# Kernel optimization log

Measured on AMD Instinct MI355X. Metric: run time of the kernel, lower is better.

Reference implementation:

```python
import jax, jax.numpy as jnp
import numpy as np

TOPK_FRAC = 0.05
TOPK_MIN = 5
TOPK_MAX = 64


def setup_inputs() -> dict:
    key = jax.random.key(0)
    ks = jax.random.split(key, 8)
    N, H, B = 131072, 256, 512
    x = jax.random.normal(ks[0], (N, H), dtype=jnp.float32)
    batch = jnp.sort(jax.random.randint(ks[1], (N,), 0, B, dtype=jnp.int32))
    W1 = jax.random.normal(ks[2], (H, H // 2), dtype=jnp.float32) * 0.05
    b1 = jax.random.normal(ks[3], (H // 2,), dtype=jnp.float32) * 0.05
    W2 = jax.random.normal(ks[4], (H // 2, 1), dtype=jnp.float32) * 0.05
    b2 = jax.random.normal(ks[5], (1,), dtype=jnp.float32) * 0.05
    Wf = jax.random.normal(ks[6], (4 * H, H), dtype=jnp.float32) * 0.05
    bf = jax.random.normal(ks[7], (H,), dtype=jnp.float32) * 0.05
    return {"x": x, "batch": batch, "W1": W1, "b1": b1, "W2": W2,
            "b2": b2, "Wf": Wf, "bf": bf, "num_graphs": B}


def _forward(x, batch, W1, b1, W2, b2, Wf, bf, B):
    N = x.shape[0]
    # attention scores per node: MLP -> scalar
    s = (jax.nn.relu(x @ W1 + b1) @ W2 + b2)[:, 0]  # [N]
    # pyg_softmax: segment-wise stable softmax over nodes of each graph
    seg_max = jax.ops.segment_max(s, batch, num_segments=B)
    seg_max = jnp.where(jnp.isfinite(seg_max), seg_max, 0.0)  # guard empty segs
    e = jnp.exp(s - seg_max[batch])
    denom = jax.ops.segment_sum(e, batch, num_segments=B)
    w = e / denom[batch]                                    # [N]
    # pools
    x_attn = jax.ops.segment_sum(x * w[:, None], batch, num_segments=B)
    counts = jax.ops.segment_sum(jnp.ones((N,), jnp.int32), batch, num_segments=B)
    cnt_f = jnp.maximum(counts, 1).astype(x.dtype)
    x_mean = jax.ops.segment_sum(x, batch, num_segments=B) / cnt_f[:, None]
    x_max = jax.ops.segment_max(x, batch, num_segments=B)
    x_max = jnp.where(counts[:, None] > 0, x_max, 0.0)
    # per-graph dynamic k
    n = counts
    k = jnp.maximum(TOPK_MIN, jnp.ceil(TOPK_FRAC * n.astype(jnp.float32)).astype(jnp.int32))
    k = jnp.minimum(jnp.minimum(k, TOPK_MAX), n)            # [B]
    # fused segment top-k mean: sort nodes by (batch asc, w desc), keep rank<k
    order = jnp.lexsort((-w, batch))
    starts = jnp.concatenate([jnp.zeros((1,), jnp.int32), jnp.cumsum(counts)[:-1].astype(jnp.int32)])
    bs = batch[order]
    rank = jnp.arange(N, dtype=jnp.int32) - starts[bs]
    sel = (rank < k[bs]).astype(x.dtype)
    x_topk = jax.ops.segment_sum(x[order] * sel[:, None], bs, num_segments=B)
    x_topk = x_topk / jnp.maximum(k, 1).astype(x.dtype)[:, None]
    g = jax.nn.relu(jnp.concatenate([x_mean, x_attn, x_max, x_topk], axis=1) @ Wf + bf)
    return g


def reference(x, batch, W1, b1, W2, b2, Wf, bf, num_graphs):
    return _forward(x, batch, W1, b1, W2, b2, Wf, bf, num_graphs)
```

## Files before the change

kernel.cpp:

```cpp
#include <hip/hip_runtime.h>
#include <math.h>

#define H 256
#define HH 128
#define B_GRAPHS 512

typedef __attribute__((ext_vector_type(8))) short bfrag8;
typedef __attribute__((ext_vector_type(16))) float f32x16;

__global__ void k_prep_w1(const float* __restrict__ W1, ushort* __restrict__ W1b) {
  const int idx = blockIdx.x * 256 + threadIdx.x;
  const int k = idx >> 7, c = idx & 127;
  const float v = W1[idx];
  const uint u = __builtin_bit_cast(uint, v);
  const float r = v - __builtin_bit_cast(float, u & 0xFFFF0000u);
  const int base = (((k >> 4) * 2 + ((k >> 3) & 1)) * 128 + c) * 8 + (k & 7);
  W1b[base] = (ushort)(u >> 16);
  W1b[32768 + base] = (ushort)(__builtin_bit_cast(uint, r) >> 16);
}

__global__ void k_seg_bounds(const int* __restrict__ batch, int* __restrict__ seg_start,
                             int N, int B) {
  int b = blockIdx.x * blockDim.x + threadIdx.x;
  if (b > B) return;
  int lo = 0, hi = N;
  while (lo < hi) {
    int mid = (lo + hi) >> 1;
    if (batch[mid] < b) lo = mid + 1; else hi = mid;
  }
  seg_start[b] = lo;
}

__device__ __forceinline__ void splitbf(const float4 v0, const float4 v1,
                                        bfrag8& a0, bfrag8& a1) {
  const float vals[8] = {v0.x, v0.y, v0.z, v0.w, v1.x, v1.y, v1.z, v1.w};
#pragma unroll
  for (int e = 0; e < 8; ++e) {
    const uint u = __builtin_bit_cast(uint, vals[e]);
    a0[e] = (short)(u >> 16);
    const float r = vals[e] - __builtin_bit_cast(float, u & 0xFFFF0000u);
    a1[e] = (short)(__builtin_bit_cast(uint, r) >> 16);
  }
}

__global__ __launch_bounds__(256, 3) void k_score_mfma(
    const float* __restrict__ x, const ushort* __restrict__ W1b,
    const float* __restrict__ b1, const float* __restrict__ W2,
    const float* __restrict__ b2, float* __restrict__ s_out) {
  __shared__ float xs[4][2192];
  const int t = threadIdx.x;
  const int lane = t & 63;
  const int w = t >> 6;
  const int nl = lane & 31, g = lane >> 5;
  const int chunk = blockIdx.x * 4 + w;
  const int node0 = chunk * 32;
  float* myxs = &xs[w][0];

  f32x16 acc[4];
  acc[0] = (f32x16)0.f; acc[1] = (f32x16)0.f;
  acc[2] = (f32x16)0.f; acc[3] = (f32x16)0.f;

  const int lrow = lane >> 4;
  const int lcol = lane & 15;
  const float* gsrc = x + (size_t)(node0 + lrow) * H + lcol * 4;

  float4 gx[8];
#pragma unroll
  for (int q = 0; q < 8; ++q)
    gx[q] = *(const float4*)(gsrc + (size_t)(q * 4) * H);

#pragma unroll
  for (int ks = 0; ks < 4; ++ks) {
#pragma unroll
    for (int q = 0; q < 8; ++q)
      *(float4*)&myxs[(q * 4 + lrow) * 68 + lcol * 4] = gx[q];
    if (ks < 3) {
#pragma unroll
      for (int q = 0; q < 8; ++q)
        gx[q] = *(const float4*)(gsrc + (size_t)(q * 4) * H + (ks + 1) * 64);
    }
#pragma unroll
    for (int sub = 0; sub < 4; ++sub) {
      const int kks = ks * 4 + sub;
      const float4 v0 = *(const float4*)&myxs[nl * 68 + sub * 16 + g * 8];
      const float4 v1 = *(const float4*)&myxs[nl * 68 + sub * 16 + g * 8 + 4];
      bfrag8 a0, a1;
      splitbf(v0, v1, a0, a1);
#pragma unroll
      for (int j = 0; j < 4; ++j) {
        const ushort* bp = W1b + (size_t)((kks * 2 + g) * 128 + j * 32 + nl) * 8;
        const bfrag8 b0 = *(const bfrag8*)bp;
        const bfrag8 b1f = *(const bfrag8*)(bp + 32768);
        acc[j] = __builtin_amdgcn_mfma_f32_32x32x16_bf16(a0, b0, acc[j], 0, 0, 0);
        acc[j] = __builtin_amdgcn_mfma_f32_32x32x16_bf16(a0, b1f, acc[j], 0, 0, 0);
        acc[j] = __builtin_amdgcn_mfma_f32_32x32x16_bf16(a1, b0, acc[j], 0, 0, 0);
      }
    }
  }

  float b1v[4], w2v[4];
#pragma unroll
  for (int j = 0; j < 4; ++j) {
    b1v[j] = b1[j * 32 + nl];
    w2v[j] = W2[j * 32 + nl];
  }
  float p[16];
#pragma unroll
  for (int r = 0; r < 16; ++r) {
    float v = 0.f;
#pragma unroll
    for (int j = 0; j < 4; ++j)
      v = fmaf(fmaxf(acc[j][r] + b1v[j], 0.f), w2v[j], v);
#pragma unroll
    for (int m = 1; m <= 16; m <<= 1) v += __shfl_xor(v, m);
    p[r] = v;
  }
  if (nl == 0) {
    const float bb = b2[0];
#pragma unroll
    for (int r = 0; r < 16; ++r) {
      const int row = (r & 3) + 8 * (r >> 2) + 4 * g;
      s_out[node0 + row] = p[r] + bb;
    }
  }
}

__global__ __launch_bounds__(512) void k_pool_fused(const float* __restrict__ x,
                                                    const float* __restrict__ s,
                                                    const int* __restrict__ seg_start,
                                                    float* __restrict__ pooled) {
  const int b = blockIdx.x;
  const int t = threadIdx.x;
  const int start = seg_start[b];
  const int end = seg_start[b + 1];
  const int n = end - start;

  __shared__ float s_lds[1024];
  __shared__ float red[512];
  __shared__ float thr_sh;
  __shared__ int thri_sh;
  __shared__ float r4[8][264];

  const bool fits = (n <= 1024);
  if (fits) {
    for (int i = t; i < n; i += 512) s_lds[i] = s[start + i];
  }
  __syncthreads();
  const float* sseg = fits ? s_lds : (s + start);

  float m = -INFINITY;
  for (int i = t; i < n; i += 512) m = fmaxf(m, sseg[i]);
  red[t] = m;
  __syncthreads();
  for (int off = 256; off > 0; off >>= 1) {
    if (t < off) red[t] = fmaxf(red[t], red[t + off]);
    __syncthreads();
  }
  const float smax = red[0];
  __syncthreads();
  float d = 0.f;
  for (int i = t; i < n; i += 512) d += __expf(sseg[i] - smax);
  red[t] = d;
  __syncthreads();
  for (int off = 256; off > 0; off >>= 1) {
    if (t < off) red[t] += red[t + off];
    __syncthreads();
  }
  const float denom = red[0];
  __syncthreads();
  const float inv_denom = (denom > 0.f) ? 1.f / denom : 0.f;

  int k = 0;
  if (n > 0) {
    k = (int)ceilf(0.05f * (float)n);
    if (k < 5) k = 5;
    if (k > 64) k = 64;
    if (k > n) k = n;
  }

  if (t < 64) {
    float pk = INFINITY;
    int pidx = -1;
    for (int r = 0; r < k; ++r) {
      float bk = -INFINITY;
      int bi = 0x7fffffff;
      for (int i = t; i < n; i += 64) {
        const float si = sseg[i];
        const int gi = start + i;
        const bool below = (si < pk) || (si == pk && gi > pidx);
        if (below && (si > bk || (si == bk && gi < bi))) { bk = si; bi = gi; }
      }
#pragma unroll
      for (int off = 32; off > 0; off >>= 1) {
        const float ok = __shfl_xor(bk, off);
        const int oi = __shfl_xor(bi, off);
        if (ok > bk || (ok == bk && oi < bi)) { bk = ok; bi = oi; }
      }
      pk = bk;
      pidx = bi;
    }
    if (t == 0) {
      thr_sh = (k > 0) ? pk : INFINITY;
      thri_sh = (k > 0) ? pidx : -1;
    }
  }
  __syncthreads();
  const float thr = thr_sh;
  const int thri = thri_sh;

  const int fq = t & 63;
  const int sub = t >> 6;
  float mean[4] = {0.f, 0.f, 0.f, 0.f};
  float attn[4] = {0.f, 0.f, 0.f, 0.f};
  float tk[4] = {0.f, 0.f, 0.f, 0.f};
  float mx[4] = {-INFINITY, -INFINITY, -INFINITY, -INFINITY};
  for (int i = sub; i < n; i += 8) {
    const float si = sseg[i];
    const float wi = __expf(si - smax);
    const int gi = start + i;
    const bool sel = (si > thr) || (si == thr && gi <= thri);
    const float4 xv = *reinterpret_cast<const float4*>(x + (size_t)gi * H + fq * 4);
    mean[0] += xv.x; mean[1] += xv.y; mean[2] += xv.z; mean[3] += xv.w;
    attn[0] = fmaf(xv.x, wi, attn[0]);
    attn[1] = fmaf(xv.y, wi, attn[1]);
    attn[2] = fmaf(xv.z, wi, attn[2]);
    attn[3] = fmaf(xv.w, wi, attn[3]);
    mx[0] = fmaxf(mx[0], xv.x);
    mx[1] = fmaxf(mx[1], xv.y);
    mx[2] = fmaxf(mx[2], xv.z);
    mx[3] = fmaxf(mx[3], xv.w);
    if (sel) {
      tk[0] += xv.x; tk[1] += xv.y; tk[2] += xv.z; tk[3] += xv.w;
    }
  }
  float* po = pooled + (size_t)b * 1024;
  const float invn = 1.f / (float)(n > 0 ? n : 1);
  const float invk = (k > 0) ? 1.f / (float)k : 0.f;
  *reinterpret_cast<float4*>(&r4[sub][fq * 4]) = make_float4(mean[0], mean[1], mean[2], mean[3]);
  __syncthreads();
  if (t < 256) {
    float tot = 0.f;
#pragma unroll
    for (int q = 0; q < 8; ++q) tot += r4[q][t];
    po[t] = tot * invn;
  }
  __syncthreads();
  *reinterpret_cast<float4*>(&r4[sub][fq * 4]) = make_float4(attn[0], attn[1], attn[2], attn[3]);
  __syncthreads();
  if (t < 256) {
    float tot = 0.f;
#pragma unroll
    for (int q = 0; q < 8; ++q) tot += r4[q][t];
    po[256 + t] = tot * inv_denom;
  }
  __syncthreads();
  *reinterpret_cast<float4*>(&r4[sub][fq * 4]) = make_float4(mx[0], mx[1], mx[2], mx[3]);
  __syncthreads();
  if (t < 256) {
    float tot = -INFINITY;
#pragma unroll
    for (int q = 0; q < 8; ++q) tot = fmaxf(tot, r4[q][t]);
    po[512 + t] = (n > 0) ? tot : 0.f;
  }
  __syncthreads();
  *reinterpret_cast<float4*>(&r4[sub][fq * 4]) = make_float4(tk[0], tk[1], tk[2], tk[3]);
  __syncthreads();
  if (t < 256) {
    float tot = 0.f;
#pragma unroll
    for (int q = 0; q < 8; ++q) tot += r4[q][t];
    po[768 + t] = tot * invk;
  }
}

__global__ __launch_bounds__(256) void k_gemm(const float* __restrict__ pooled,
                                              const float* __restrict__ Wf,
                                              float* __restrict__ gacc) {
  const int t = threadIdx.x;
  const int r0 = blockIdx.x * 8;
  const int kc0 = blockIdx.y * 128;
  __shared__ float ps[8][132];
  {
    const int r = t >> 5;
    const int c = (t & 31) << 2;
    *reinterpret_cast<float4*>(&ps[r][c]) =
        *reinterpret_cast<const float4*>(pooled + (size_t)(r0 + r) * 1024 + kc0 + c);
  }
  __syncthreads();
  float acc[8];
#pragma unroll
  for (int r = 0; r < 8; ++r) acc[r] = 0.f;
#pragma unroll 4
  for (int c = 0; c < 128; ++c) {
    const float wf = Wf[(size_t)(kc0 + c) * 256 + t];
#pragma unroll
    for (int r = 0; r < 8; ++r) acc[r] = fmaf(ps[r][c], wf, acc[r]);
  }
  float* go = gacc + ((size_t)blockIdx.y * B_GRAPHS + r0) * 256;
#pragma unroll
  for (int r = 0; r < 8; ++r) go[r * 256 + t] = acc[r];
}

__global__ __launch_bounds__(256) void k_out(const float* __restrict__ gacc,
                                             const float* __restrict__ bf,
                                             float* __restrict__ out) {
  const int i = blockIdx.x * 256 + threadIdx.x;
  float v = bf[i & 255];
#pragma unroll
  for (int ks = 0; ks < 8; ++ks) v += gacc[(size_t)ks * (B_GRAPHS * 256) + i];
  out[i] = fmaxf(v, 0.f);
}

extern "C" void kernel_launch(void* const* d_in, const int* in_sizes, int n_in,
                              void* d_out, int out_size, void* d_ws, size_t ws_size,
                              hipStream_t stream) {
  const float* x  = (const float*)d_in[0];
  const int* batch = (const int*)d_in[1];
  const float* W1 = (const float*)d_in[2];
  const float* b1 = (const float*)d_in[3];
  const float* W2 = (const float*)d_in[4];
  const float* b2 = (const float*)d_in[5];
  const float* Wf = (const float*)d_in[6];
  const float* bf = (const float*)d_in[7];
  const int N = in_sizes[1];
  const int B = B_GRAPHS;

  float* ws = (float*)d_ws;
  float* s = ws;
  int* seg_start = (int*)(ws + N);
  float* pooled = ws + N + 1024;
  float* gacc = pooled + (size_t)B * 1024;
  ushort* W1b = (ushort*)(gacc + (size_t)8 * B * 256);

  k_prep_w1<<<dim3(128), dim3(256), 0, stream>>>(W1, W1b);
  k_seg_bounds<<<dim3((B + 1 + 255) / 256), dim3(256), 0, stream>>>(batch, seg_start, N, B);
  k_score_mfma<<<dim3(N / 128), dim3(256), 0, stream>>>(x, W1b, b1, W2, b2, s);
  k_pool_fused<<<dim3(B), dim3(512), 0, stream>>>(x, s, seg_start, pooled);
  k_gemm<<<dim3(B / 8, 8), dim3(256), 0, stream>>>(pooled, Wf, gacc);
  k_out<<<dim3((B * 256) / 256), dim3(256), 0, stream>>>(gacc, bf, (float*)d_out);
}
```

Baseline: 110.4 us.

## Split score GEMM K-dimension across warps with LDS partial-sum reduction

The score kernel previously gave each wavefront 32 nodes and looped over the full K=256, staging x through shared memory. Now each block handles 32 nodes and its four wavefronts each take a quarter of K, loading x directly into registers. The partial accumulators are then reduced through shared memory before the ReLU/W2 epilogue. This gives four times more blocks and shorter per-wave dependency chains, at the cost of extra LDS traffic and two block barriers.

```diff
diff --git a/kernel.cpp b/kernel.cpp
--- a/kernel.cpp
+++ b/kernel.cpp
@@ -47,81 +47,81 @@
     const float* __restrict__ x, const ushort* __restrict__ W1b,
     const float* __restrict__ b1, const float* __restrict__ W2,
     const float* __restrict__ b2, float* __restrict__ s_out) {
-  __shared__ float xs[4][2192];
+  __shared__ float part[4][16][128];
   const int t = threadIdx.x;
   const int lane = t & 63;
   const int w = t >> 6;
   const int nl = lane & 31, g = lane >> 5;
-  const int chunk = blockIdx.x * 4 + w;
-  const int node0 = chunk * 32;
-  float* myxs = &xs[w][0];
+  const int node0 = blockIdx.x * 32;
 
   f32x16 acc[4];
   acc[0] = (f32x16)0.f; acc[1] = (f32x16)0.f;
   acc[2] = (f32x16)0.f; acc[3] = (f32x16)0.f;
 
-  const int lrow = lane >> 4;
-  const int lcol = lane & 15;
-  const float* gsrc = x + (size_t)(node0 + lrow) * H + lcol * 4;
-
-  float4 gx[8];
-#pragma unroll
-  for (int q = 0; q < 8; ++q)
-    gx[q] = *(const float4*)(gsrc + (size_t)(q * 4) * H);
-
-#pragma unroll
-  for (int ks = 0; ks < 4; ++ks) {
-#pragma unroll
-    for (int q = 0; q < 8; ++q)
-      *(float4*)&myxs[(q * 4 + lrow) * 68 + lcol * 4] = gx[q];
-    if (ks < 3) {
-#pragma unroll
-      for (int q = 0; q < 8; ++q)
-        gx[q] = *(const float4*)(gsrc + (size_t)(q * 4) * H + (ks + 1) * 64);
-    }
-#pragma unroll
-    for (int sub = 0; sub < 4; ++sub) {
-      const int kks = ks * 4 + sub;
-      const float4 v0 = *(const float4*)&myxs[nl * 68 + sub * 16 + g * 8];
-      const float4 v1 = *(const float4*)&myxs[nl * 68 + sub * 16 + g * 8 + 4];
-      bfrag8 a0, a1;
-      splitbf(v0, v1, a0, a1);
-#pragma unroll
-      for (int j = 0; j < 4; ++j) {
-        const ushort* bp = W1b + (size_t)((kks * 2 + g) * 128 + j * 32 + nl) * 8;
-        const bfrag8 b0 = *(const bfrag8*)bp;
-        const bfrag8 b1f = *(const bfrag8*)(bp + 32768);
-        acc[j] = __builtin_amdgcn_mfma_f32_32x32x16_bf16(a0, b0, acc[j], 0, 0, 0);
-        acc[j] = __builtin_amdgcn_mfma_f32_32x32x16_bf16(a0, b1f, acc[j], 0, 0, 0);
-        acc[j] = __builtin_amdgcn_mfma_f32_32x32x16_bf16(a1, b0, acc[j], 0, 0, 0);
+  const float* gsrc = x + (size_t)(node0 + nl) * H + w * 64 + g * 8;
+  float4 xv[4][2];
+#pragma unroll
+  for (int sub = 0; sub < 4; ++sub) {
+    xv[sub][0] = *(const float4*)(gsrc + sub * 16);
+    xv[sub][1] = *(const float4*)(gsrc + sub * 16 + 4);
+  }
+
+#pragma unroll
+  for (int sub = 0; sub < 4; ++sub) {
+    const int kks = w * 4 + sub;
+    bfrag8 a0, a1;
+    splitbf(xv[sub][0], xv[sub][1], a0, a1);
+#pragma unroll
+    for (int j = 0; j < 4; ++j) {
+      const ushort* bp = W1b + (size_t)((kks * 2 + g) * 128 + j * 32 + nl) * 8;
+      const bfrag8 b0 = *(const bfrag8*)bp;
+      const bfrag8 b1f = *(const bfrag8*)(bp + 32768);
+      acc[j] = __builtin_amdgcn_mfma_f32_32x32x16_bf16(a0, b0, acc[j], 0, 0, 0);
+      acc[j] = __builtin_amdgcn_mfma_f32_32x32x16_bf16(a0, b1f, acc[j], 0, 0, 0);
+      acc[j] = __builtin_amdgcn_mfma_f32_32x32x16_bf16(a1, b0, acc[j], 0, 0, 0);
+    }
+  }
+
+  const float b2v = b2[0];
+  const int hb = (t & 15) * 8;
+  const int nloc = t >> 4;
+  float b1q[8], w2q[8];
+#pragma unroll
+  for (int e = 0; e < 8; ++e) {
+    b1q[e] = b1[hb + e];
+    w2q[e] = W2[hb + e];
+  }
+
+#pragma unroll
+  for (int P = 0; P < 2; ++P) {
+#pragma unroll
+    for (int j = 0; j < 4; ++j)
+#pragma unroll
+      for (int rr = 0; rr < 8; ++rr) {
+        const int nd = (rr & 3) + 8 * (rr >> 2) + 4 * g;
+        part[w][nd][j * 32 + nl] = acc[j][P * 8 + rr];
       }
-    }
-  }
-
-  float b1v[4], w2v[4];
-#pragma unroll
-  for (int j = 0; j < 4; ++j) {
-    b1v[j] = b1[j * 32 + nl];
-    w2v[j] = W2[j * 32 + nl];
-  }
-  float p[16];
-#pragma unroll
-  for (int r = 0; r < 16; ++r) {
+    __syncthreads();
+    float h8[8];
+#pragma unroll
+    for (int e = 0; e < 8; e += 4) {
+      const float4 s0 = *(const float4*)&part[0][nloc][hb + e];
+      const float4 s1 = *(const float4*)&part[1][nloc][hb + e];
+      const float4 s2 = *(const float4*)&part[2][nloc][hb + e];
+      const float4 s3 = *(const float4*)&part[3][nloc][hb + e];
+      h8[e + 0] = s0.x + s1.x + s2.x + s3.x;
+      h8[e + 1] = s0.y + s1.y + s2.y + s3.y;
+      h8[e + 2] = s0.z + s1.z + s2.z + s3.z;
+      h8[e + 3] = s0.w + s1.w + s2.w + s3.w;
+    }
     float v = 0.f;
 #pragma unroll
-    for (int j = 0; j < 4; ++j)
-      v = fmaf(fmaxf(acc[j][r] + b1v[j], 0.f), w2v[j], v);
-#pragma unroll
-    for (int m = 1; m <= 16; m <<= 1) v += __shfl_xor(v, m);
-    p[r] = v;
-  }
-  if (nl == 0) {
-    const float bb = b2[0];
-#pragma unroll
-    for (int r = 0; r < 16; ++r) {
-      const int row = (r & 3) + 8 * (r >> 2) + 4 * g;
-      s_out[node0 + row] = p[r] + bb;
-    }
+    for (int e = 0; e < 8; ++e)
+      v = fmaf(fmaxf(h8[e] + b1q[e], 0.f), w2q[e], v);
+#pragma unroll
+    for (int m = 1; m < 16; m <<= 1) v += __shfl_xor(v, m);
+    if ((t & 15) == 0) s_out[node0 + P * 16 + nloc] = v + b2v;
+    if (P == 0) __syncthreads();
   }
 }
 
@@ -334,7 +334,7 @@
 
   k_prep_w1<<<dim3(128), dim3(256), 0, stream>>>(W1, W1b);
   k_seg_bounds<<<dim3((B + 1 + 255) / 256), dim3(256), 0, stream>>>(batch, seg_start, N, B);
-  k_score_mfma<<<dim3(N / 128), dim3(256), 0, stream>>>(x, W1b, b1, W2, b2, s);
+  k_score_mfma<<<dim3(N / 32), dim3(256), 0, stream>>>(x, W1b, b1, W2, b2, s);
   k_pool_fused<<<dim3(B), dim3(512), 0, stream>>>(x, s, seg_start, pooled);
   k_gemm<<<dim3(B / 8, 8), dim3(256), 0, stream>>>(pooled, Wf, gacc);
   k_out<<<dim3((B * 256) / 256), dim3(256), 0, stream>>>(gacc, bf, (float*)d_out);
```

Result: no change. 111.0 us (+0.5%).

## Stage split-bf16 W1 in LDS and stream x directly into registers

Applied to the files above, without the earlier changes.

The score kernel now uses 1024-thread blocks that first copy the whole hi/lo bf16 W1 (128 KB) into dynamic shared memory. MFMA B-fragments are then read from LDS instead of global memory. The x rows are loaded straight from global into registers with a double-buffered prefetch, replacing the old per-wave LDS staging of x. The aim is to cut repeated global/L2 traffic for W1 and the x LDS round trip. The costs are one block per CU, a large per-block W1 preload, less coalesced x loads, and a tight launch-bounds register budget.

```diff
diff --git a/kernel.cpp b/kernel.cpp
--- a/kernel.cpp
+++ b/kernel.cpp
@@ -43,57 +43,68 @@
   }
 }
 
-__global__ __launch_bounds__(256, 3) void k_score_mfma(
+__global__ __launch_bounds__(1024, 4) void k_score_mfma(
     const float* __restrict__ x, const ushort* __restrict__ W1b,
     const float* __restrict__ b1, const float* __restrict__ W2,
     const float* __restrict__ b2, float* __restrict__ s_out) {
-  __shared__ float xs[4][2192];
+  extern __shared__ ushort bsh[];
   const int t = threadIdx.x;
   const int lane = t & 63;
   const int w = t >> 6;
   const int nl = lane & 31, g = lane >> 5;
-  const int chunk = blockIdx.x * 4 + w;
+
+  {
+    const uint4* src = (const uint4*)W1b + t * 8;
+    uint4* dst = (uint4*)bsh + t * 8;
+#pragma unroll
+    for (int i = 0; i < 8; ++i) dst[i] = src[i];
+  }
+  __syncthreads();
+
+  const int chunk = blockIdx.x * 16 + w;
   const int node0 = chunk * 32;
-  float* myxs = &xs[w][0];
+  const float* gsrc = x + (size_t)(node0 + nl) * H + g * 8;
 
   f32x16 acc[4];
   acc[0] = (f32x16)0.f; acc[1] = (f32x16)0.f;
   acc[2] = (f32x16)0.f; acc[3] = (f32x16)0.f;
 
-  const int lrow = lane >> 4;
-  const int lcol = lane & 15;
-  const float* gsrc = x + (size_t)(node0 + lrow) * H + lcol * 4;
-
-  float4 gx[8];
-#pragma unroll
-  for (int q = 0; q < 8; ++q)
-    gx[q] = *(const float4*)(gsrc + (size_t)(q * 4) * H);
-
-#pragma unroll
-  for (int ks = 0; ks < 4; ++ks) {
-#pragma unroll
-    for (int q = 0; q < 8; ++q)
-      *(float4*)&myxs[(q * 4 + lrow) * 68 + lcol * 4] = gx[q];
-    if (ks < 3) {
-#pragma unroll
-      for (int q = 0; q < 8; ++q)
-        gx[q] = *(const float4*)(gsrc + (size_t)(q * 4) * H + (ks + 1) * 64);
-    }
-#pragma unroll
-    for (int sub = 0; sub < 4; ++sub) {
-      const int kks = ks * 4 + sub;
-      const float4 v0 = *(const float4*)&myxs[nl * 68 + sub * 16 + g * 8];
-      const float4 v1 = *(const float4*)&myxs[nl * 68 + sub * 16 + g * 8 + 4];
+  float4 xa[2][2], xb[2][2];
+#pragma unroll
+  for (int q = 0; q < 2; ++q) {
+    xa[q][0] = *(const float4*)(gsrc + q * 16);
+    xa[q][1] = *(const float4*)(gsrc + q * 16 + 4);
+  }
+
+#pragma unroll
+  for (int pair = 0; pair < 8; ++pair) {
+    if (pair < 7) {
+#pragma unroll
+      for (int q = 0; q < 2; ++q) {
+        xb[q][0] = *(const float4*)(gsrc + ((pair + 1) * 2 + q) * 16);
+        xb[q][1] = *(const float4*)(gsrc + ((pair + 1) * 2 + q) * 16 + 4);
+      }
+    }
+#pragma unroll
+    for (int q = 0; q < 2; ++q) {
+      const int kks = pair * 2 + q;
       bfrag8 a0, a1;
-      splitbf(v0, v1, a0, a1);
+      splitbf(xa[q][0], xa[q][1], a0, a1);
 #pragma unroll
       for (int j = 0; j < 4; ++j) {
-        const ushort* bp = W1b + (size_t)((kks * 2 + g) * 128 + j * 32 + nl) * 8;
+        const ushort* bp = &bsh[(size_t)((kks * 2 + g) * 128 + j * 32 + nl) * 8];
         const bfrag8 b0 = *(const bfrag8*)bp;
         const bfrag8 b1f = *(const bfrag8*)(bp + 32768);
         acc[j] = __builtin_amdgcn_mfma_f32_32x32x16_bf16(a0, b0, acc[j], 0, 0, 0);
         acc[j] = __builtin_amdgcn_mfma_f32_32x32x16_bf16(a0, b1f, acc[j], 0, 0, 0);
         acc[j] = __builtin_amdgcn_mfma_f32_32x32x16_bf16(a1, b0, acc[j], 0, 0, 0);
+      }
+    }
+    if (pair < 7) {
+#pragma unroll
+      for (int q = 0; q < 2; ++q) {
+        xa[q][0] = xb[q][0];
+        xa[q][1] = xb[q][1];
       }
     }
   }
@@ -332,9 +343,16 @@
   float* gacc = pooled + (size_t)B * 1024;
   ushort* W1b = (ushort*)(gacc + (size_t)8 * B * 256);
 
+  static bool attr_set = false;
+  if (!attr_set) {
+    hipFuncSetAttribute((const void*)k_score_mfma,
+                        hipFuncAttributeMaxDynamicSharedMemorySize, 131072);
+    attr_set = true;
+  }
+
   k_prep_w1<<<dim3(128), dim3(256), 0, stream>>>(W1, W1b);
   k_seg_bounds<<<dim3((B + 1 + 255) / 256), dim3(256), 0, stream>>>(batch, seg_start, N, B);
-  k_score_mfma<<<dim3(N / 128), dim3(256), 0, stream>>>(x, W1b, b1, W2, b2, s);
+  k_score_mfma<<<dim3(N / 512), dim3(1024), 131072, stream>>>(x, W1b, b1, W2, b2, s);
   k_pool_fused<<<dim3(B), dim3(512), 0, stream>>>(x, s, seg_start, pooled);
   k_gemm<<<dim3(B / 8, 8), dim3(256), 0, stream>>>(pooled, Wf, gacc);
   k_out<<<dim3((B * 256) / 256), dim3(256), 0, stream>>>(gacc, bf, (float*)d_out);
```

Measured after the change: 108.0 us. 2.2% less time.
